# Kernel optimization log

Hardware: AMD Instinct MI355X
Metric: run time of the kernel (lower is better)

## Reference

```python
import jax, jax.numpy as jnp
import numpy as np

N, B, T, C = 4096, 64, 512, 4
STD = 1.0 / np.sqrt(N)
SAT_LO, SAT_HI = 0.0, 1.0e6  # ReLU-clamp saturations


def setup_inputs() -> dict:
    key = jax.random.key(0)
    k0, k1, k2, k3 = jax.random.split(key, 4)
    inputs = jax.random.normal(k0, (C, B, T), dtype=jnp.float32)
    state = jnp.zeros((B, N), dtype=jnp.float32)
    mask = jnp.ones((N,), dtype=jnp.float32)
    W = jax.random.normal(k1, (N, N), dtype=jnp.float32) * STD
    encoders = jax.random.normal(k2, (C, N), dtype=jnp.float32) * STD
    bias_current = jnp.zeros((N,), dtype=jnp.float32)
    dec_w = jax.random.normal(k3, (C, N), dtype=jnp.float32) * STD
    dec_b = jnp.zeros((C,), dtype=jnp.float32)
    return {"inputs": inputs, "state": state, "mask": mask, "W": W,
            "encoders": encoders, "bias_current": bias_current,
            "dec_w": dec_w, "dec_b": dec_b}


def reference(inputs, state, mask, W, encoders, bias_current, dec_w, dec_b):
    act = lambda x: jnp.clip(x, SAT_LO, SAT_HI)
    xs = jnp.transpose(inputs, (2, 0, 1))  # [T, C, B]

    def step(s, x_t):
        # external current: sum over channels of encoders[i] * input_i  -> [B, N]
        ext = jnp.einsum('cb,cn->bn', x_t, encoders)
        s_new = mask * (bias_current + act((s + mask * ext) @ W.T))  # [B, N]
        out = act(s_new @ dec_w.T + dec_b)  # decode -> [B, C]
        return s_new, out

    _, outs = jax.lax.scan(step, state, xs)  # outs: [T, B, C]
    return jnp.transpose(outs, (2, 1, 0))    # [C, B, T] (matches permute(1,0,2))
```

## Files before the change

kernel.cpp:

```cpp
#include <hip/hip_runtime.h>
#include <stdint.h>

typedef __attribute__((ext_vector_type(8))) short short8;
typedef __attribute__((ext_vector_type(4))) float fl4;
typedef __attribute__((ext_vector_type(2))) float fl2;
typedef __attribute__((ext_vector_type(8))) unsigned short us8;

#define SAT_HI 1.0e6f
#define ZSLOT 262144u

__device__ __forceinline__ unsigned short f2bf(float f) {
  unsigned u = __float_as_uint(f);
  u += 0x7fffu + ((u >> 16) & 1u);
  return (unsigned short)(u >> 16);
}
__device__ __forceinline__ float clipf(float x) {
  return fminf(fmaxf(x, 0.0f), SAT_HI);
}

__device__ __forceinline__ void gload16(const void* g, void* l) {
  __builtin_amdgcn_global_load_lds(
      (const __attribute__((address_space(1))) void*)g,
      (__attribute__((address_space(3))) void*)l, 16, 0, 0);
}

__device__ __forceinline__ void stage_chunk(const char* zsrc, char* dst,
                                            int rows0, int h, int lane) {
#pragma unroll
  for (int i = 0; i < 8; ++i) {
    const int rl = 2 * i + (lane >> 5);
    const unsigned q = (unsigned)(lane & 31) ^ ((unsigned)rl & 7u);
    gload16(zsrc + (size_t)(rows0 + rl) * 8192 + h * 512 + (q << 4),
            dst + i * 1024);
  }
}

__device__ __forceinline__ void gwait(const int* pgc, int target) {
  while (__hip_atomic_load(pgc, __ATOMIC_RELAXED, __HIP_MEMORY_SCOPE_AGENT) < target)
    __builtin_amdgcn_s_sleep(1);
  __builtin_amdgcn_sched_barrier(0);
}

#define MFMA_CHUNK(BUF, H, ACCA, ACCB)                                         \
  _Pragma("unroll")                                                            \
  for (int ki_ = 0; ki_ < 8; ++ki_) {                                          \
    short8 a_ = *(const short8*)((BUF) + lo * 512 +                            \
        ((((unsigned)(ki_ * 4 + hi)) ^ ((unsigned)lo & 7u)) << 4));            \
    ACCA = __builtin_amdgcn_mfma_f32_16x16x32_bf16(a_, wf[(H) * 8 + ki_], ACCA, 0, 0, 0); \
    ACCB = __builtin_amdgcn_mfma_f32_16x16x32_bf16(a_, wf[16 + (H) * 8 + ki_], ACCB, 0, 0, 0); \
  }

__global__ __launch_bounds__(256) void prep_kernel(const float* __restrict__ W,
                                                   unsigned short* __restrict__ wfrag) {
  unsigned u = blockIdx.x * 256u + threadIdx.x;
  unsigned lane = u & 63u, lo = lane & 15u, hi = lane >> 4;
  unsigned ki = (u >> 6) & 15u;
  unsigned cf = (u >> 10) & 1u;
  unsigned w = (u >> 11) & 7u;
  unsigned ct = u >> 14;
  unsigned n = ct * 32u + cf * 16u + lo;
  unsigned k = w * 512u + ki * 32u + hi * 8u;
  const float* src = W + (size_t)n * 4096u + k;
  fl4 s0 = *(const fl4*)(src);
  fl4 s1 = *(const fl4*)(src + 4);
  us8 o;
  o[0] = f2bf(s0[0]); o[1] = f2bf(s0[1]); o[2] = f2bf(s0[2]); o[3] = f2bf(s0[3]);
  o[4] = f2bf(s1[0]); o[5] = f2bf(s1[1]); o[6] = f2bf(s1[2]); o[7] = f2bf(s1[3]);
  *(us8*)(wfrag + (size_t)u * 8u) = o;
}

__global__ __launch_bounds__(512, 2) void persist_kernel(
    const float* __restrict__ xin,
    const float* __restrict__ state0,
    const float* __restrict__ mask,
    const float* __restrict__ enc,
    const float* __restrict__ bias,
    const float* __restrict__ decw,
    const unsigned short* __restrict__ wfrag,
    unsigned short* __restrict__ zbuf,
    float* __restrict__ dsc8,
    int* __restrict__ cnt,
    int R, int invP) {
  __shared__ __align__(16) unsigned char sm[131072];
  __shared__ float decbuf[8][32][4];

  const int tid = threadIdx.x;
  const int wave = tid >> 6;
  const int lane = tid & 63;
  const int lo = lane & 15, hi = lane >> 4;
  const int g = blockIdx.x;
  const int rt = g & 1;
  const int ct = g >> 1;
  float* dscg = dsc8 + (size_t)(ct & 7) * 131072u;
  int* mypgc = cnt + (rt * 8 + (ct >> 4)) * 32;
  int* wpgc  = cnt + (rt * 8 + wave) * 32;

  short8 wf[32];
  {
    const short8* wp = (const short8*)wfrag + (size_t)(ct * 8 + wave) * 32u * 64u + lane;
#pragma unroll
    for (int f = 0; f < 32; ++f) wf[f] = wp[(size_t)f * 64u];
  }

  const int r = tid >> 4, c2 = (tid & 15) * 2;
  const int b = rt * 32 + r;
  const int n0 = ct * 32 + c2;
  const fl2 mk = *(const fl2*)(mask + n0);
  const fl2 bi = *(const fl2*)(bias + n0);
  const fl2 e0 = *(const fl2*)(enc + n0);
  const fl2 e1 = *(const fl2*)(enc + 4096 + n0);
  const fl2 e2 = *(const fl2*)(enc + 8192 + n0);
  const fl2 e3 = *(const fl2*)(enc + 12288 + n0);
  const fl2 w0 = *(const fl2*)(decw + n0);
  const fl2 w1 = *(const fl2*)(decw + 4096 + n0);
  const fl2 w2 = *(const fl2*)(decw + 8192 + n0);
  const fl2 w3 = *(const fl2*)(decw + 12288 + n0);
  const float* xp = xin + b * 512;
  const size_t kwb = (size_t)wave * 1024u;
  const int rbase = rt * 32;

  char* buf0 = (char*)sm + wave * 16384;
  char* buf1 = buf0 + 8192;
  float* pown = (float*)buf0;

  {
    fl2 st = *(const fl2*)(state0 + (size_t)b * 4096u + n0);
    float x0 = xp[0], x1 = xp[32768], x2 = xp[65536], x3 = xp[98304];
    float z0 = st[0] + mk[0] * (x0 * e0[0] + x1 * e1[0] + x2 * e2[0] + x3 * e3[0]);
    float z1 = st[1] + mk[1] * (x0 * e0[1] + x1 * e1[1] + x2 * e2[1] + x3 * e3[1]);
    unsigned pack = (unsigned)f2bf(z0) | ((unsigned)f2bf(z1) << 16);
    __hip_atomic_store((unsigned*)(zbuf + (size_t)b * 4096u + n0), pack,
                       __ATOMIC_RELAXED, __HIP_MEMORY_SCOPE_SYSTEM);
  }
  __syncthreads();
  if (tid == 0)
    __hip_atomic_fetch_add(mypgc, 1, __ATOMIC_RELAXED, __HIP_MEMORY_SCOPE_AGENT);

  int cur = 0;
  int invc = invP;
  for (int t = 0; t < 512; ++t) {
    float xv0 = 0.f, xv1 = 0.f, xv2 = 0.f, xv3 = 0.f;
    if (t < 511) {
      xv0 = xp[t + 1]; xv1 = xp[32768 + t + 1];
      xv2 = xp[65536 + t + 1]; xv3 = xp[98304 + t + 1];
    }

    gwait(wpgc, 16 * (t + 1));
    const char* zsrc = (const char*)(zbuf + (size_t)cur * ZSLOT) + kwb;

    fl4 a00 = {0.f,0.f,0.f,0.f}, a01 = a00, a10 = a00, a11 = a00;
    stage_chunk(zsrc, buf0, rbase, 0, lane);
    stage_chunk(zsrc, buf1, rbase + 16, 0, lane);
    asm volatile("s_waitcnt vmcnt(8)" ::: "memory");
    __builtin_amdgcn_sched_barrier(0);
    MFMA_CHUNK(buf0, 0, a00, a01);
    asm volatile("s_waitcnt lgkmcnt(0)" ::: "memory");
    __builtin_amdgcn_sched_barrier(0);
    stage_chunk(zsrc, buf0, rbase, 1, lane);
    asm volatile("s_waitcnt vmcnt(8)" ::: "memory");
    __builtin_amdgcn_sched_barrier(0);
    MFMA_CHUNK(buf1, 0, a10, a11);
    asm volatile("s_waitcnt lgkmcnt(0)" ::: "memory");
    __builtin_amdgcn_sched_barrier(0);
    stage_chunk(zsrc, buf1, rbase + 16, 1, lane);
    asm volatile("s_waitcnt vmcnt(8)" ::: "memory");
    __builtin_amdgcn_sched_barrier(0);
    MFMA_CHUNK(buf0, 1, a00, a01);
    asm volatile("s_waitcnt vmcnt(0)" ::: "memory");
    __builtin_amdgcn_sched_barrier(0);
    MFMA_CHUNK(buf1, 1, a10, a11);
    asm volatile("s_waitcnt lgkmcnt(0)" ::: "memory");
    __builtin_amdgcn_sched_barrier(0);

#pragma unroll
    for (int rr = 0; rr < 4; ++rr) {
      pown[(hi * 4 + rr) * 36 + lo] = a00[rr];
      pown[(hi * 4 + rr) * 36 + 16 + lo] = a01[rr];
      pown[(16 + hi * 4 + rr) * 36 + lo] = a10[rr];
      pown[(16 + hi * 4 + rr) * 36 + 16 + lo] = a11[rr];
    }
    __syncthreads();

    float y0 = 0.f, y1 = 0.f;
#pragma unroll
    for (int w = 0; w < 8; ++w) {
      fl2 v = *(const fl2*)((const char*)sm + w * 16384 + (size_t)(r * 36 + c2) * 4u);
      y0 += v[0]; y1 += v[1];
    }
    float sn0 = mk[0] * (bi[0] + clipf(y0));
    float sn1 = mk[1] * (bi[1] + clipf(y1));

    if (t < 511) {
      int ns = cur + 1; if (ns == R) ns = 0;
      float z0 = sn0 + mk[0] * (xv0 * e0[0] + xv1 * e1[0] + xv2 * e2[0] + xv3 * e3[0]);
      float z1 = sn1 + mk[1] * (xv0 * e0[1] + xv1 * e1[1] + xv2 * e2[1] + xv3 * e3[1]);
      unsigned pack = (unsigned)f2bf(z0) | ((unsigned)f2bf(z1) << 16);
      __hip_atomic_store((unsigned*)(zbuf + (size_t)ns * ZSLOT + (size_t)b * 4096u + n0),
                         pack, __ATOMIC_RELAXED, __HIP_MEMORY_SCOPE_SYSTEM);
      cur = ns;
    }
    __syncthreads();

    if (t < 511 && tid == 0) {
      __hip_atomic_fetch_add(mypgc, 1, __ATOMIC_RELAXED, __HIP_MEMORY_SCOPE_AGENT);
      if (--invc == 0) {
        invc = invP;
        (void)__hip_atomic_load(mypgc, __ATOMIC_ACQUIRE, __HIP_MEMORY_SCOPE_AGENT);
      }
    }

    float d0 = sn0 * w0[0] + sn1 * w0[1];
    float d1 = sn0 * w1[0] + sn1 * w1[1];
    float d2 = sn0 * w2[0] + sn1 * w2[1];
    float d3 = sn0 * w3[0] + sn1 * w3[1];
    d0 += __shfl_xor(d0, 1); d0 += __shfl_xor(d0, 2); d0 += __shfl_xor(d0, 4); d0 += __shfl_xor(d0, 8);
    d1 += __shfl_xor(d1, 1); d1 += __shfl_xor(d1, 2); d1 += __shfl_xor(d1, 4); d1 += __shfl_xor(d1, 8);
    d2 += __shfl_xor(d2, 1); d2 += __shfl_xor(d2, 2); d2 += __shfl_xor(d2, 4); d2 += __shfl_xor(d2, 8);
    d3 += __shfl_xor(d3, 1); d3 += __shfl_xor(d3, 2); d3 += __shfl_xor(d3, 4); d3 += __shfl_xor(d3, 8);
    if ((tid & 15) < 4) {
      const int ch = tid & 3;
      float dv = d0;
      if (ch == 1) dv = d1; else if (ch == 2) dv = d2; else if (ch == 3) dv = d3;
      decbuf[t & 7][r][ch] = dv;
    }
    if ((t & 7) == 7) {
      __syncthreads();
      if (tid < 128) {
        const int row = tid >> 2, ch = tid & 3;
        float* dp = dscg + ch * 32768 + (rbase + row) * 512 + (t - 7);
#pragma unroll
        for (int j = 0; j < 8; ++j)
          atomicAdd(dp + j, decbuf[j][row][ch]);
      }
    }
  }
}

__global__ __launch_bounds__(256) void final_kernel(const float* __restrict__ dsc8,
                                                    const float* __restrict__ decb,
                                                    float* __restrict__ out) {
  const unsigned u = blockIdx.x * 256u + threadIdx.x;
  const unsigned c = u >> 15;
  float s = decb[c];
#pragma unroll
  for (int g = 0; g < 8; ++g) s += dsc8[(size_t)g * 131072u + u];
  out[u] = clipf(s);
}

extern "C" void kernel_launch(void* const* d_in, const int* in_sizes, int n_in,
                              void* d_out, int out_size, void* d_ws, size_t ws_size,
                              hipStream_t stream) {
  const float* xin  = (const float*)d_in[0];
  const float* st   = (const float*)d_in[1];
  const float* mask = (const float*)d_in[2];
  const float* W    = (const float*)d_in[3];
  const float* enc  = (const float*)d_in[4];
  const float* bias = (const float*)d_in[5];
  const float* decw = (const float*)d_in[6];
  const float* decb = (const float*)d_in[7];
  char* ws = (char*)d_ws;

  const size_t WFRAG_B = 33554432ull;
  const size_t SLOT_B  = 524288ull;
  const size_t DSC_B   = 4194304ull;
  const size_t CNT_B   = 4096ull;
  const size_t fixed   = WFRAG_B + DSC_B + CNT_B;

  int R = 4;
  if (ws_size > fixed) {
    size_t r = (ws_size - fixed) / SLOT_B;
    R = (r > 256) ? 256 : (int)r;
    if (R < 4) R = 4;
  }
  const int invP = R - 3;

  unsigned short* wfrag = (unsigned short*)(ws);
  unsigned short* zbuf  = (unsigned short*)(ws + WFRAG_B);
  float* dsc8 = (float*)(ws + WFRAG_B + (size_t)R * SLOT_B);
  int* cnt    = (int*)(ws + WFRAG_B + (size_t)R * SLOT_B + DSC_B);

  hipMemsetAsync(cnt, 0, CNT_B, stream);
  hipMemsetAsync(dsc8, 0, DSC_B, stream);
  prep_kernel<<<8192, 256, 0, stream>>>(W, wfrag);
  persist_kernel<<<256, 512, 0, stream>>>(xin, st, mask, enc, bias, decw,
                                          wfrag, zbuf, dsc8, cnt, R, invP);
  final_kernel<<<512, 256, 0, stream>>>(dsc8, decb, (float*)d_out);
}
```

Before: 3.864 ms.

## Load activation fragments directly into registers and split progress counters per half

Replaces the LDS staging of z activations (global_load_lds with swizzled layout and double-buffered waits) with direct per-lane 16-byte global loads into registers that feed the MFMAs. It shrinks shared memory to just the reduction scratch, which may allow better occupancy, and splits each progress counter into two finer-grained counters that each wave waits on separately. This removes LDS round-trips and the manual waitcnt pipelining. In exchange it uses more registers for the 16 preloaded fragments and issues strided uncoalesced global loads, with less overlap between loads and MFMAs.

```diff
diff --git a/kernel.cpp b/kernel.cpp
--- a/kernel.cpp
+++ b/kernel.cpp
@@ -18,37 +18,11 @@
   return fminf(fmaxf(x, 0.0f), SAT_HI);
 }
 
-__device__ __forceinline__ void gload16(const void* g, void* l) {
-  __builtin_amdgcn_global_load_lds(
-      (const __attribute__((address_space(1))) void*)g,
-      (__attribute__((address_space(3))) void*)l, 16, 0, 0);
-}
-
-__device__ __forceinline__ void stage_chunk(const char* zsrc, char* dst,
-                                            int rows0, int h, int lane) {
-#pragma unroll
-  for (int i = 0; i < 8; ++i) {
-    const int rl = 2 * i + (lane >> 5);
-    const unsigned q = (unsigned)(lane & 31) ^ ((unsigned)rl & 7u);
-    gload16(zsrc + (size_t)(rows0 + rl) * 8192 + h * 512 + (q << 4),
-            dst + i * 1024);
-  }
-}
-
 __device__ __forceinline__ void gwait(const int* pgc, int target) {
   while (__hip_atomic_load(pgc, __ATOMIC_RELAXED, __HIP_MEMORY_SCOPE_AGENT) < target)
     __builtin_amdgcn_s_sleep(1);
   __builtin_amdgcn_sched_barrier(0);
 }
-
-#define MFMA_CHUNK(BUF, H, ACCA, ACCB)                                         \
-  _Pragma("unroll")                                                            \
-  for (int ki_ = 0; ki_ < 8; ++ki_) {                                          \
-    short8 a_ = *(const short8*)((BUF) + lo * 512 +                            \
-        ((((unsigned)(ki_ * 4 + hi)) ^ ((unsigned)lo & 7u)) << 4));            \
-    ACCA = __builtin_amdgcn_mfma_f32_16x16x32_bf16(a_, wf[(H) * 8 + ki_], ACCA, 0, 0, 0); \
-    ACCB = __builtin_amdgcn_mfma_f32_16x16x32_bf16(a_, wf[16 + (H) * 8 + ki_], ACCB, 0, 0, 0); \
-  }
 
 __global__ __launch_bounds__(256) void prep_kernel(const float* __restrict__ W,
                                                    unsigned short* __restrict__ wfrag) {
@@ -81,7 +55,7 @@
     float* __restrict__ dsc8,
     int* __restrict__ cnt,
     int R, int invP) {
-  __shared__ __align__(16) unsigned char sm[131072];
+  __shared__ float pown[8][32][36];
   __shared__ float decbuf[8][32][4];
 
   const int tid = threadIdx.x;
@@ -92,8 +66,9 @@
   const int rt = g & 1;
   const int ct = g >> 1;
   float* dscg = dsc8 + (size_t)(ct & 7) * 131072u;
-  int* mypgc = cnt + (rt * 8 + (ct >> 4)) * 32;
-  int* wpgc  = cnt + (rt * 8 + wave) * 32;
+  int* mypgc = cnt + (rt * 16 + (ct >> 4) * 2 + ((ct >> 3) & 1)) * 32;
+  int* wpgcA = cnt + (rt * 16 + wave * 2) * 32;
+  int* wpgcB = wpgcA + 32;
 
   short8 wf[32];
   {
@@ -116,12 +91,8 @@
   const fl2 w2 = *(const fl2*)(decw + 8192 + n0);
   const fl2 w3 = *(const fl2*)(decw + 12288 + n0);
   const float* xp = xin + b * 512;
-  const size_t kwb = (size_t)wave * 1024u;
+  const size_t kwb = (size_t)wave * 1024u + (size_t)hi * 16u;
   const int rbase = rt * 32;
-
-  char* buf0 = (char*)sm + wave * 16384;
-  char* buf1 = buf0 + 8192;
-  float* pown = (float*)buf0;
 
   {
     fl2 st = *(const fl2*)(state0 + (size_t)b * 4096u + n0);
@@ -145,46 +116,45 @@
       xv2 = xp[65536 + t + 1]; xv3 = xp[98304 + t + 1];
     }
 
-    gwait(wpgc, 16 * (t + 1));
-    const char* zsrc = (const char*)(zbuf + (size_t)cur * ZSLOT) + kwb;
+    gwait(wpgcA, 8 * (t + 1));
+    gwait(wpgcB, 8 * (t + 1));
+    const char* zs = (const char*)(zbuf + (size_t)cur * ZSLOT) + kwb;
+    asm volatile("" : "+v"(zs));
 
     fl4 a00 = {0.f,0.f,0.f,0.f}, a01 = a00, a10 = a00, a11 = a00;
-    stage_chunk(zsrc, buf0, rbase, 0, lane);
-    stage_chunk(zsrc, buf1, rbase + 16, 0, lane);
-    asm volatile("s_waitcnt vmcnt(8)" ::: "memory");
-    __builtin_amdgcn_sched_barrier(0);
-    MFMA_CHUNK(buf0, 0, a00, a01);
-    asm volatile("s_waitcnt lgkmcnt(0)" ::: "memory");
-    __builtin_amdgcn_sched_barrier(0);
-    stage_chunk(zsrc, buf0, rbase, 1, lane);
-    asm volatile("s_waitcnt vmcnt(8)" ::: "memory");
-    __builtin_amdgcn_sched_barrier(0);
-    MFMA_CHUNK(buf1, 0, a10, a11);
-    asm volatile("s_waitcnt lgkmcnt(0)" ::: "memory");
-    __builtin_amdgcn_sched_barrier(0);
-    stage_chunk(zsrc, buf1, rbase + 16, 1, lane);
-    asm volatile("s_waitcnt vmcnt(8)" ::: "memory");
-    __builtin_amdgcn_sched_barrier(0);
-    MFMA_CHUNK(buf0, 1, a00, a01);
-    asm volatile("s_waitcnt vmcnt(0)" ::: "memory");
-    __builtin_amdgcn_sched_barrier(0);
-    MFMA_CHUNK(buf1, 1, a10, a11);
-    asm volatile("s_waitcnt lgkmcnt(0)" ::: "memory");
-    __builtin_amdgcn_sched_barrier(0);
+    {
+      short8 a[16];
+#pragma unroll
+      for (int kk = 0; kk < 16; ++kk)
+        a[kk] = *(const short8*)(zs + (size_t)(rbase + lo) * 8192u + kk * 64);
+#pragma unroll
+      for (int kk = 0; kk < 16; ++kk) {
+        a00 = __builtin_amdgcn_mfma_f32_16x16x32_bf16(a[kk], wf[kk], a00, 0, 0, 0);
+        a01 = __builtin_amdgcn_mfma_f32_16x16x32_bf16(a[kk], wf[16 + kk], a01, 0, 0, 0);
+      }
+#pragma unroll
+      for (int kk = 0; kk < 16; ++kk)
+        a[kk] = *(const short8*)(zs + (size_t)(rbase + 16 + lo) * 8192u + kk * 64);
+#pragma unroll
+      for (int kk = 0; kk < 16; ++kk) {
+        a10 = __builtin_amdgcn_mfma_f32_16x16x32_bf16(a[kk], wf[kk], a10, 0, 0, 0);
+        a11 = __builtin_amdgcn_mfma_f32_16x16x32_bf16(a[kk], wf[16 + kk], a11, 0, 0, 0);
+      }
+    }
 
 #pragma unroll
     for (int rr = 0; rr < 4; ++rr) {
-      pown[(hi * 4 + rr) * 36 + lo] = a00[rr];
-      pown[(hi * 4 + rr) * 36 + 16 + lo] = a01[rr];
-      pown[(16 + hi * 4 + rr) * 36 + lo] = a10[rr];
-      pown[(16 + hi * 4 + rr) * 36 + 16 + lo] = a11[rr];
+      pown[wave][hi * 4 + rr][lo] = a00[rr];
+      pown[wave][hi * 4 + rr][16 + lo] = a01[rr];
+      pown[wave][16 + hi * 4 + rr][lo] = a10[rr];
+      pown[wave][16 + hi * 4 + rr][16 + lo] = a11[rr];
     }
     __syncthreads();
 
     float y0 = 0.f, y1 = 0.f;
 #pragma unroll
     for (int w = 0; w < 8; ++w) {
-      fl2 v = *(const fl2*)((const char*)sm + w * 16384 + (size_t)(r * 36 + c2) * 4u);
+      fl2 v = *(const fl2*)(&pown[w][r][c2]);
       y0 += v[0]; y1 += v[1];
     }
     float sn0 = mk[0] * (bi[0] + clipf(y0));
```

After: 5.310 ms. 37.4% more time.
